# Optimization experiments

Measured on AMD Instinct MI355X. Metric: run time of the kernel, lower is better.

## Reference

```python
import jax, jax.numpy as jnp
import numpy as np

C = 16        # channel_n
HID = 128     # hidden width of 1x1 MLP
FIRE_RATE = 0.5
STEP_SIZE = 1.0
ALIVE_THRESH = 0.1
B, H, W = 16, 256, 256


def _perceive_kernel():
    # identity + Sobel filters, angle = 0.0 so cos=1, sin=0
    ident = np.outer([0.0, 1.0, 0.0], [0.0, 1.0, 0.0]).astype(np.float32)
    dxk = (np.outer([1.0, 2.0, 1.0], [-1.0, 0.0, 1.0]) / 8.0).astype(np.float32)
    dyk = dxk.T
    k3 = np.stack([ident, dxk, dyk], axis=-1)  # [3,3,3]
    # TF depthwise layout: out channel index = c*3 + k  -> tile over channels
    rhs = np.tile(k3, (1, 1, C)).reshape(3, 3, 1, 3 * C)  # HWIO, groups=C
    return jnp.asarray(rhs)


def _get_living_mask(x):
    alpha = x[:, :, :, 3:4]
    pooled = jax.lax.reduce_window(alpha, -jnp.inf, jax.lax.max,
                                   (1, 3, 3, 1), (1, 1, 1, 1), 'SAME')
    return pooled > ALIVE_THRESH


def _perceive(x):
    rhs = _perceive_kernel()
    return jax.lax.conv_general_dilated(
        x, rhs, window_strides=(1, 1), padding='SAME',
        dimension_numbers=('NHWC', 'HWIO', 'NHWC'),
        feature_group_count=C)  # [B,H,W,3C]


def setup_inputs() -> dict:
    key = jax.random.key(0)
    kx, kw1, kb1, ku = jax.random.split(key, 4)
    x = jax.random.normal(kx, (B, H, W, C), dtype=jnp.float32)
    # dmodel params: Conv2D(128,1,relu) then Conv2D(16,1,zeros init); use
    # random values for a meaningful numeric baseline
    W1 = jax.random.normal(kw1, (3 * C, HID), dtype=jnp.float32) * 0.1
    b1 = jax.random.normal(kb1, (HID,), dtype=jnp.float32) * 0.01
    W2 = jax.random.normal(jax.random.fold_in(key, 7), (HID, C), dtype=jnp.float32) * 0.1
    b2 = jnp.zeros((C,), dtype=jnp.float32)
    rand_u = jax.random.uniform(ku, (B, H, W, 1), dtype=jnp.float32)
    return {"x": x, "W1": W1, "b1": b1, "W2": W2, "b2": b2, "rand_u": rand_u}


def reference(x, W1, b1, W2, b2, rand_u):
    pre_life_mask = _get_living_mask(x)
    y = _perceive(x)                                         # [B,H,W,48]
    h = jax.nn.relu(jnp.einsum('bhwc,cd->bhwd', y, W1) + b1)  # [B,H,W,128]
    dx = (jnp.einsum('bhwd,dc->bhwc', h, W2) + b2) * STEP_SIZE
    update_mask = (rand_u <= FIRE_RATE).astype(x.dtype)
    x = x + dx * update_mask
    post_life_mask = _get_living_mask(x)
    life_mask = (pre_life_mask & post_life_mask).astype(x.dtype)
    return x * life_mask
```

## Files before the change

kernel.cpp:

```cpp
#include <hip/hip_runtime.h>


#define NC 16
#define NHID 128
#define NPIX (16 * 256 * 256)
#define MG 0.04f
#define MAXFIX 65536

typedef __attribute__((ext_vector_type(8))) short s8b;
typedef __attribute__((ext_vector_type(4))) float f4;

__device__ __forceinline__ unsigned short f2bf(float f) {
    union { float f; unsigned int u; } v; v.f = f;
    unsigned int r = (v.u + 0x7FFFu + ((v.u >> 16) & 1u)) >> 16;
    return (unsigned short)r;
}
__device__ __forceinline__ unsigned int pack2(float a, float b) {
    return (unsigned int)f2bf(a) | ((unsigned int)f2bf(b) << 16);
}

__global__ __launch_bounds__(256) void ca_prep(
    const float* __restrict__ W1, const float* __restrict__ b1,
    const float* __restrict__ W2, uint4* __restrict__ w1p, uint4* __restrict__ w2p)
{
    const int tid = threadIdx.x;
    if (blockIdx.x == 0) {
        for (int idx = tid; idx < 1024; idx += 256) {
            const int fid = idx >> 6, lane = idx & 63;
            const int k0 = fid >> 3, mt = fid & 7;
            const int q = lane >> 4, i = lane & 15;
            unsigned int u[4];
            #pragma unroll
            for (int jp = 0; jp < 4; ++jp) {
                int k = k0 * 32 + q * 8 + jp * 2;
                float v0 = (k < 48) ? W1[k * 128 + mt * 16 + i] : ((k == 48) ? b1[mt * 16 + i] : 0.f);
                k++;
                float v1 = (k < 48) ? W1[k * 128 + mt * 16 + i] : ((k == 48) ? b1[mt * 16 + i] : 0.f);
                u[jp] = pack2(v0, v1);
            }
            w1p[idx] = make_uint4(u[0], u[1], u[2], u[3]);
        }
    } else {
        for (int idx = tid; idx < 256; idx += 256) {
            const int k2 = idx >> 6, lane = idx & 63;
            const int q = lane >> 4, i = lane & 15;
            unsigned int u[4];
            #pragma unroll
            for (int jp = 0; jp < 4; ++jp) {
                const int k = k2 * 32 + q * 8 + jp * 2;
                u[jp] = pack2(W2[k * 16 + i], W2[(k + 1) * 16 + i]);
            }
            w2p[idx] = make_uint4(u[0], u[1], u[2], u[3]);
        }
    }
}

__global__ __launch_bounds__(256, 3) void ca_update(
    const float* __restrict__ x, const float* __restrict__ b2,
    const float* __restrict__ rand_u, const uint4* __restrict__ w1p,
    const uint4* __restrict__ w2p, float* __restrict__ out,
    float* __restrict__ ws_alpha, unsigned char* __restrict__ ws_pre,
    unsigned int* __restrict__ fix_cnt, unsigned int* __restrict__ fix_list)
{
    __shared__ __align__(16) float xw[18 * 18 * 20];
    __shared__ __align__(16) unsigned short yfs[4 * 2 * 528];
    __shared__ float lsr[256];

    const int tid  = threadIdx.x;
    const int lane = tid & 63;
    const int li   = lane & 15;
    const int lq   = lane >> 4;
    const int wv   = tid >> 6;
    const int tx   = tid & 15, ty = tid >> 4;
    const int w0 = blockIdx.x * 16, h0 = blockIdx.y * 16, bb = blockIdx.z;

    float b2v[4];
    #pragma unroll
    for (int r = 0; r < 4; ++r) b2v[r] = b2[lq * 4 + r];

    for (int i = tid; i < 324; i += 256) {
        const int ly = i / 18, lx = i - ly * 18;
        const int gh = h0 + ly - 1, gw = w0 + lx - 1;
        float4 v0, v1, v2, v3;
        if (gh >= 0 && gh < 256 && gw >= 0 && gw < 256) {
            const float4* p = (const float4*)(x + (((size_t)bb * 256 + gh) * 256 + gw) * NC);
            v0 = p[0]; v1 = p[1]; v2 = p[2]; v3 = p[3];
        } else {
            v0 = v1 = v2 = v3 = make_float4(0.f, 0.f, 0.f, 0.f);
        }
        float4* t = (float4*)(xw + i * 20);
        t[0] = v0; t[1] = v1; t[2] = v2; t[3] = v3;
    }
    const size_t gpix = ((size_t)bb * 256 + h0 + ty) * 256 + (w0 + tx);
    lsr[tid] = rand_u[gpix];
    __syncthreads();

    const int o_mm = ((ty + 0) * 18 + tx + 0) * 20, o_m0 = ((ty + 0) * 18 + tx + 1) * 20, o_mp = ((ty + 0) * 18 + tx + 2) * 20;
    const int o_0m = ((ty + 1) * 18 + tx + 0) * 20, o_cc = ((ty + 1) * 18 + tx + 1) * 20, o_0p = ((ty + 1) * 18 + tx + 2) * 20;
    const int o_pm = ((ty + 2) * 18 + tx + 0) * 20, o_p0 = ((ty + 2) * 18 + tx + 1) * 20, o_pp = ((ty + 2) * 18 + tx + 2) * 20;

    float am = xw[o_mm + 3];
    am = fmaxf(am, xw[o_m0 + 3]); am = fmaxf(am, xw[o_mp + 3]);
    am = fmaxf(am, xw[o_0m + 3]); am = fmaxf(am, xw[o_cc + 3]); am = fmaxf(am, xw[o_0p + 3]);
    am = fmaxf(am, xw[o_pm + 3]); am = fmaxf(am, xw[o_p0 + 3]); am = fmaxf(am, xw[o_pp + 3]);
    ws_pre[gpix] = (am > 0.1f) ? (unsigned char)1 : (unsigned char)0;

    unsigned int yu[24];
    #pragma unroll
    for (int cq = 0; cq < 4; ++cq) {
        const int co = cq * 4;
        float4 vmm = *(const float4*)(xw + o_mm + co); const float* pmm = (const float*)&vmm;
        float4 vm0 = *(const float4*)(xw + o_m0 + co); const float* pm0 = (const float*)&vm0;
        float4 vmp = *(const float4*)(xw + o_mp + co); const float* pmp = (const float*)&vmp;
        float4 v0m = *(const float4*)(xw + o_0m + co); const float* p0m = (const float*)&v0m;
        float4 vcc = *(const float4*)(xw + o_cc + co); const float* pcc = (const float*)&vcc;
        float4 v0p = *(const float4*)(xw + o_0p + co); const float* p0p = (const float*)&v0p;
        float4 vpm = *(const float4*)(xw + o_pm + co); const float* ppm = (const float*)&vpm;
        float4 vp0 = *(const float4*)(xw + o_p0 + co); const float* pp0 = (const float*)&vp0;
        float4 vpp = *(const float4*)(xw + o_pp + co); const float* ppp = (const float*)&vpp;
        float yl[12];
        #pragma unroll
        for (int cc = 0; cc < 4; ++cc) {
            const float xmm = pmm[cc], xm0 = pm0[cc], xmp = pmp[cc];
            const float x0m = p0m[cc], xcc = pcc[cc], x0p = p0p[cc];
            const float xpm = ppm[cc], xp0 = pp0[cc], xpp = ppp[cc];
            yl[cc * 3 + 0] = xcc;
            yl[cc * 3 + 1] = ((xmp - xmm) + 2.f * (x0p - x0m) + (xpp - xpm)) * 0.125f;
            yl[cc * 3 + 2] = ((xpm - xmm) + 2.f * (xp0 - xm0) + (xpp - xmp)) * 0.125f;
        }
        #pragma unroll
        for (int m2 = 0; m2 < 6; ++m2) yu[cq * 6 + m2] = pack2(yl[2 * m2], yl[2 * m2 + 1]);
    }

    float4 xcr[4];
    #pragma unroll
    for (int s4 = 0; s4 < 4; ++s4)
        xcr[s4] = *(const float4*)(xw + ((wv * 4 + s4 + 1) * 18 + li + 1) * 20 + lq * 4);
    __syncthreads();

    for (int i = tid; i < 1280; i += 256)
        ((uint4*)xw)[i] = w1p[i];
    __syncthreads();

    const unsigned short* wl = (const unsigned short*)xw;
    unsigned short* yfw = yfs + wv * (2 * 528);

    const int srcA = li + (lq & 1) * 32;
    const int srcB = srcA + 16;
    const bool hiq = (lq >= 2);

    #pragma unroll
    for (int s = 0; s < 4; ++s) {
        const int t = wv * 4 + s;
        if ((ty & 3) == s) {
            #pragma unroll
            for (int q = 0; q < 4; ++q)
                *(uint4*)(yfw + (q * 16 + tx) * 8) = make_uint4(yu[q * 4], yu[q * 4 + 1], yu[q * 4 + 2], yu[q * 4 + 3]);
            *(uint4*)(yfw + 528 + (0 * 16 + tx) * 8) = make_uint4(yu[16], yu[17], yu[18], yu[19]);
            *(uint4*)(yfw + 528 + (1 * 16 + tx) * 8) = make_uint4(yu[20], yu[21], yu[22], yu[23]);
            *(uint4*)(yfw + 528 + (2 * 16 + tx) * 8) = make_uint4(0x3F80u, 0u, 0u, 0u);
            *(uint4*)(yfw + 528 + (3 * 16 + tx) * 8) = make_uint4(0u, 0u, 0u, 0u);
        }
        const s8b ya0 = *(const s8b*)(yfw + lane * 8);
        const s8b ya1 = *(const s8b*)(yfw + 528 + lane * 8);

        f4 acc1[8];
        #pragma unroll
        for (int mt = 0; mt < 8; ++mt) { f4 z = {0.f, 0.f, 0.f, 0.f}; acc1[mt] = z; }
        #pragma unroll
        for (int mt = 0; mt < 8; ++mt) {
            const s8b wf = *(const s8b*)(wl + mt * 512 + lane * 8);
            acc1[mt] = __builtin_amdgcn_mfma_f32_16x16x32_bf16(wf, ya0, acc1[mt], 0, 0, 0);
        }
        #pragma unroll
        for (int mt = 0; mt < 8; ++mt) {
            const s8b wf = *(const s8b*)(wl + (8 + mt) * 512 + lane * 8);
            acc1[mt] = __builtin_amdgcn_mfma_f32_16x16x32_bf16(wf, ya1, acc1[mt], 0, 0, 0);
        }

        f4 acc2[2];
        { f4 z = {0.f, 0.f, 0.f, 0.f}; acc2[0] = z; acc2[1] = z; }
        #pragma unroll
        for (int k2 = 0; k2 < 4; ++k2) {
            const f4 aE = acc1[2 * k2], aO = acc1[2 * k2 + 1];
            const unsigned int e0 = pack2(fmaxf(aE[0], 0.f), fmaxf(aE[1], 0.f));
            const unsigned int e1 = pack2(fmaxf(aE[2], 0.f), fmaxf(aE[3], 0.f));
            const unsigned int o0 = pack2(fmaxf(aO[0], 0.f), fmaxf(aO[1], 0.f));
            const unsigned int o1 = pack2(fmaxf(aO[2], 0.f), fmaxf(aO[3], 0.f));
            const unsigned int vE0A = (unsigned int)__shfl((int)e0, srcA, 64);
            const unsigned int vE1A = (unsigned int)__shfl((int)e1, srcA, 64);
            const unsigned int vO0A = (unsigned int)__shfl((int)o0, srcA, 64);
            const unsigned int vO1A = (unsigned int)__shfl((int)o1, srcA, 64);
            const unsigned int vE0B = (unsigned int)__shfl((int)e0, srcB, 64);
            const unsigned int vE1B = (unsigned int)__shfl((int)e1, srcB, 64);
            const unsigned int vO0B = (unsigned int)__shfl((int)o0, srcB, 64);
            const unsigned int vO1B = (unsigned int)__shfl((int)o1, srcB, 64);
            union { uint4 u; s8b v; } hb;
            hb.u = make_uint4(hiq ? vO0A : vE0A, hiq ? vO1A : vE1A,
                              hiq ? vO0B : vE0B, hiq ? vO1B : vE1B);
            const s8b w2fr = *(const s8b*)(wl + 8192 + k2 * 512 + lane * 8);
            acc2[k2 >> 1] = __builtin_amdgcn_mfma_f32_16x16x32_bf16(w2fr, hb.v, acc2[k2 >> 1], 0, 0, 0);
        }

        const float um = (lsr[t * 16 + li] <= 0.5f) ? 1.f : 0.f;
        const size_t gp = ((size_t)bb * 256 + h0 + t) * 256 + (w0 + li);
        const float4 xc = xcr[s];
        f4 nx;
        nx[0] = fmaf(acc2[0][0] + acc2[1][0] + b2v[0], um, xc.x);
        nx[1] = fmaf(acc2[0][1] + acc2[1][1] + b2v[1], um, xc.y);
        nx[2] = fmaf(acc2[0][2] + acc2[1][2] + b2v[2], um, xc.z);
        nx[3] = fmaf(acc2[0][3] + acc2[1][3] + b2v[3], um, xc.w);
        __builtin_nontemporal_store(nx, (f4*)out + gp * 4 + lq);
        if (lq == 0) {
            ws_alpha[gp] = nx[3];
            if (um != 0.f && fabsf(nx[3] - 0.1f) <= MG) {
                unsigned int idx = atomicAdd(fix_cnt, 1u);
                if (idx < MAXFIX) fix_list[idx] = (unsigned int)gp;
            }
        }
    }
}

__global__ __launch_bounds__(64) void ca_fix(
    const float* __restrict__ x, const float* __restrict__ W1,
    const float* __restrict__ b1, const float* __restrict__ W2,
    const float* __restrict__ b2,
    const unsigned int* __restrict__ fix_cnt, const unsigned int* __restrict__ fix_list,
    float* __restrict__ ws_alpha)
{
    __shared__ float ysh[48];
    const int lane = threadIdx.x;
    unsigned int n = *fix_cnt;
    if (n > MAXFIX) n = MAXFIX;
    for (unsigned int e = blockIdx.x; e < n; e += gridDim.x) {
        const unsigned int pix = fix_list[e];
        const int bb = pix >> 16, h = (pix >> 8) & 255, w = pix & 255;
        if (lane < 48) {
            const int c = lane / 3, j = lane - c * 3;
            float v = 0.f;
            #pragma unroll
            for (int dy = 0; dy < 3; ++dy) {
                #pragma unroll
                for (int dxx = 0; dxx < 3; ++dxx) {
                    const int hh = h + dy - 1, ww = w + dxx - 1;
                    if (hh < 0 || hh >= 256 || ww < 0 || ww >= 256) continue;
                    const float f = x[(((size_t)bb * 256 + hh) * 256 + ww) * 16 + c];
                    float wgt;
                    if (j == 0) wgt = (dy == 1 && dxx == 1) ? 1.f : 0.f;
                    else if (j == 1) wgt = ((dy == 1) ? 2.f : 1.f) * (float)(dxx - 1) * 0.125f;
                    else wgt = ((dxx == 1) ? 2.f : 1.f) * (float)(dy - 1) * 0.125f;
                    v = fmaf(f, wgt, v);
                }
            }
            ysh[lane] = v;
        }
        __syncthreads();
        float dot = 0.f;
        #pragma unroll
        for (int t = 0; t < 2; ++t) {
            const int d = t * 64 + lane;
            float a = b1[d];
            #pragma unroll
            for (int k = 0; k < 48; ++k)
                a = fmaf(ysh[k], W1[k * 128 + d], a);
            dot = fmaf(fmaxf(a, 0.f), W2[d * 16 + 3], dot);
        }
        #pragma unroll
        for (int off = 32; off > 0; off >>= 1)
            dot += __shfl_down(dot, off, 64);
        if (lane == 0)
            ws_alpha[pix] = x[(size_t)pix * 16 + 3] + dot + b2[3];
        __syncthreads();
    }
}

__global__ __launch_bounds__(256) void ca_mask(
    const float* __restrict__ alpha, const unsigned char* __restrict__ pre,
    float* __restrict__ out)
{
    __shared__ float at[18 * 20];
    const int tid = threadIdx.x;
    const int w0 = blockIdx.x * 16, h0 = blockIdx.y * 16, bb = blockIdx.z;
    for (int i = tid; i < 324; i += 256) {
        const int ly = i / 18, lx = i - ly * 18;
        const int gh = h0 + ly - 1, gw = w0 + lx - 1;
        float v = 0.f;
        if (gh >= 0 && gh < 256 && gw >= 0 && gw < 256)
            v = alpha[((size_t)bb * 256 + gh) * 256 + gw];
        at[ly * 20 + lx] = v;
    }
    __syncthreads();
    const int txx = tid & 15, tyy = tid >> 4;
    float m = at[tyy * 20 + txx];
    m = fmaxf(m, at[tyy * 20 + txx + 1]); m = fmaxf(m, at[tyy * 20 + txx + 2]);
    m = fmaxf(m, at[(tyy + 1) * 20 + txx]); m = fmaxf(m, at[(tyy + 1) * 20 + txx + 1]); m = fmaxf(m, at[(tyy + 1) * 20 + txx + 2]);
    m = fmaxf(m, at[(tyy + 2) * 20 + txx]); m = fmaxf(m, at[(tyy + 2) * 20 + txx + 1]); m = fmaxf(m, at[(tyy + 2) * 20 + txx + 2]);
    const size_t gp = ((size_t)bb * 256 + h0 + tyy) * 256 + (w0 + txx);
    const bool alive = (m > 0.1f) && pre[gp];
    if (!alive) {
        float4* po = (float4*)(out + gp * 16);
        const float4 z = make_float4(0.f, 0.f, 0.f, 0.f);
        po[0] = z; po[1] = z; po[2] = z; po[3] = z;
    }
}

extern "C" void kernel_launch(void* const* d_in, const int* in_sizes, int n_in,
                              void* d_out, int out_size, void* d_ws, size_t ws_size,
                              hipStream_t stream) {
    (void)in_sizes; (void)n_in; (void)out_size; (void)ws_size;
    const float* x  = (const float*)d_in[0];
    const float* W1 = (const float*)d_in[1];
    const float* b1 = (const float*)d_in[2];
    const float* W2 = (const float*)d_in[3];
    const float* b2 = (const float*)d_in[4];
    const float* ru = (const float*)d_in[5];
    float* out = (float*)d_out;

    char* ws = (char*)d_ws;
    float* ws_alpha       = (float*)ws;
    unsigned char* ws_pre = (unsigned char*)(ws + (size_t)NPIX * 4);
    uint4* w1p            = (uint4*)(ws + (size_t)NPIX * 5);
    uint4* w2p            = w1p + 1024;
    unsigned int* fix_cnt = (unsigned int*)(ws + (size_t)NPIX * 5 + 20480);
    unsigned int* fix_list= fix_cnt + 4;

    (void)hipMemsetAsync(fix_cnt, 0, sizeof(unsigned int), stream);
    ca_prep<<<2, 256, 0, stream>>>(W1, b1, W2, w1p, w2p);
    dim3 g(16, 16, 16);
    ca_update<<<g, 256, 0, stream>>>(x, b2, ru, w1p, w2p, out, ws_alpha, ws_pre, fix_cnt, fix_list);
    ca_fix<<<4096, 64, 0, stream>>>(x, W1, b1, W2, b2, fix_cnt, fix_list, ws_alpha);
    ca_mask<<<g, 256, 0, stream>>>(ws_alpha, ws_pre, out);
}
```

Baseline: 340.2 us.

## Read stencil neighbors directly from global memory instead of LDS halo tile

Removes the 18x18x20 float shared-memory halo tile. Each thread now loads its nine neighbor pixels straight from global memory through the cache, and the center pixel and rand_u are re-read from global in the epilogue. The W1 weight copy into shared memory moves to the kernel start, which drops one barrier and a large chunk of LDS, so more blocks can be resident per CU. The cost is roughly nine times more global or cache load traffic per pixel, instead of one halo-tile load per block.

```diff
diff --git a/kernel.cpp b/kernel.cpp
--- a/kernel.cpp
+++ b/kernel.cpp
@@ -62,9 +62,8 @@
     float* __restrict__ ws_alpha, unsigned char* __restrict__ ws_pre,
     unsigned int* __restrict__ fix_cnt, unsigned int* __restrict__ fix_list)
 {
-    __shared__ __align__(16) float xw[18 * 18 * 20];
+    __shared__ __align__(16) uint4 wsm[1280];
     __shared__ __align__(16) unsigned short yfs[4 * 2 * 528];
-    __shared__ float lsr[256];
 
     const int tid  = threadIdx.x;
     const int lane = tid & 63;
@@ -74,50 +73,57 @@
     const int tx   = tid & 15, ty = tid >> 4;
     const int w0 = blockIdx.x * 16, h0 = blockIdx.y * 16, bb = blockIdx.z;
 
+    for (int i = tid; i < 1280; i += 256)
+        wsm[i] = w1p[i];
+
     float b2v[4];
     #pragma unroll
     for (int r = 0; r < 4; ++r) b2v[r] = b2[lq * 4 + r];
 
-    for (int i = tid; i < 324; i += 256) {
-        const int ly = i / 18, lx = i - ly * 18;
-        const int gh = h0 + ly - 1, gw = w0 + lx - 1;
-        float4 v0, v1, v2, v3;
-        if (gh >= 0 && gh < 256 && gw >= 0 && gw < 256) {
-            const float4* p = (const float4*)(x + (((size_t)bb * 256 + gh) * 256 + gw) * NC);
-            v0 = p[0]; v1 = p[1]; v2 = p[2]; v3 = p[3];
-        } else {
-            v0 = v1 = v2 = v3 = make_float4(0.f, 0.f, 0.f, 0.f);
-        }
-        float4* t = (float4*)(xw + i * 20);
-        t[0] = v0; t[1] = v1; t[2] = v2; t[3] = v3;
-    }
-    const size_t gpix = ((size_t)bb * 256 + h0 + ty) * 256 + (w0 + tx);
-    lsr[tid] = rand_u[gpix];
-    __syncthreads();
-
-    const int o_mm = ((ty + 0) * 18 + tx + 0) * 20, o_m0 = ((ty + 0) * 18 + tx + 1) * 20, o_mp = ((ty + 0) * 18 + tx + 2) * 20;
-    const int o_0m = ((ty + 1) * 18 + tx + 0) * 20, o_cc = ((ty + 1) * 18 + tx + 1) * 20, o_0p = ((ty + 1) * 18 + tx + 2) * 20;
-    const int o_pm = ((ty + 2) * 18 + tx + 0) * 20, o_p0 = ((ty + 2) * 18 + tx + 1) * 20, o_pp = ((ty + 2) * 18 + tx + 2) * 20;
-
-    float am = xw[o_mm + 3];
-    am = fmaxf(am, xw[o_m0 + 3]); am = fmaxf(am, xw[o_mp + 3]);
-    am = fmaxf(am, xw[o_0m + 3]); am = fmaxf(am, xw[o_cc + 3]); am = fmaxf(am, xw[o_0p + 3]);
-    am = fmaxf(am, xw[o_pm + 3]); am = fmaxf(am, xw[o_p0 + 3]); am = fmaxf(am, xw[o_pp + 3]);
-    ws_pre[gpix] = (am > 0.1f) ? (unsigned char)1 : (unsigned char)0;
+    const int gh = h0 + ty, gw = w0 + tx;
+    const size_t gpix = ((size_t)bb * 256 + gh) * 256 + gw;
+    const float* xb = x + (size_t)bb * 256 * 256 * NC;
+
+    bool nv[3][3];
+    size_t nb[3][3];
+    #pragma unroll
+    for (int dy = 0; dy < 3; ++dy) {
+        const int hh = gh + dy - 1;
+        const bool hv = (hh >= 0) && (hh < 256);
+        #pragma unroll
+        for (int dxx = 0; dxx < 3; ++dxx) {
+            const int ww = gw + dxx - 1;
+            nv[dy][dxx] = hv && (ww >= 0) && (ww < 256);
+            nb[dy][dxx] = ((size_t)(hv ? hh : 0) * 256 + (size_t)((ww >= 0 && ww < 256) ? ww : 0)) * NC;
+        }
+    }
 
     unsigned int yu[24];
+    float am = 0.f;
     #pragma unroll
     for (int cq = 0; cq < 4; ++cq) {
         const int co = cq * 4;
-        float4 vmm = *(const float4*)(xw + o_mm + co); const float* pmm = (const float*)&vmm;
-        float4 vm0 = *(const float4*)(xw + o_m0 + co); const float* pm0 = (const float*)&vm0;
-        float4 vmp = *(const float4*)(xw + o_mp + co); const float* pmp = (const float*)&vmp;
-        float4 v0m = *(const float4*)(xw + o_0m + co); const float* p0m = (const float*)&v0m;
-        float4 vcc = *(const float4*)(xw + o_cc + co); const float* pcc = (const float*)&vcc;
-        float4 v0p = *(const float4*)(xw + o_0p + co); const float* p0p = (const float*)&v0p;
-        float4 vpm = *(const float4*)(xw + o_pm + co); const float* ppm = (const float*)&vpm;
-        float4 vp0 = *(const float4*)(xw + o_p0 + co); const float* pp0 = (const float*)&vp0;
-        float4 vpp = *(const float4*)(xw + o_pp + co); const float* ppp = (const float*)&vpp;
+        const float4 z4 = make_float4(0.f, 0.f, 0.f, 0.f);
+        float4 vmm = nv[0][0] ? *(const float4*)(xb + nb[0][0] + co) : z4;
+        float4 vm0 = nv[0][1] ? *(const float4*)(xb + nb[0][1] + co) : z4;
+        float4 vmp = nv[0][2] ? *(const float4*)(xb + nb[0][2] + co) : z4;
+        float4 v0m = nv[1][0] ? *(const float4*)(xb + nb[1][0] + co) : z4;
+        float4 vcc = nv[1][1] ? *(const float4*)(xb + nb[1][1] + co) : z4;
+        float4 v0p = nv[1][2] ? *(const float4*)(xb + nb[1][2] + co) : z4;
+        float4 vpm = nv[2][0] ? *(const float4*)(xb + nb[2][0] + co) : z4;
+        float4 vp0 = nv[2][1] ? *(const float4*)(xb + nb[2][1] + co) : z4;
+        float4 vpp = nv[2][2] ? *(const float4*)(xb + nb[2][2] + co) : z4;
+        if (cq == 0) {
+            am = vmm.w;
+            am = fmaxf(am, vm0.w); am = fmaxf(am, vmp.w);
+            am = fmaxf(am, v0m.w); am = fmaxf(am, vcc.w); am = fmaxf(am, v0p.w);
+            am = fmaxf(am, vpm.w); am = fmaxf(am, vp0.w); am = fmaxf(am, vpp.w);
+        }
+        const float* pmm = (const float*)&vmm; const float* pm0 = (const float*)&vm0;
+        const float* pmp = (const float*)&vmp; const float* p0m = (const float*)&v0m;
+        const float* pcc = (const float*)&vcc; const float* p0p = (const float*)&v0p;
+        const float* ppm = (const float*)&vpm; const float* pp0 = (const float*)&vp0;
+        const float* ppp = (const float*)&vpp;
         float yl[12];
         #pragma unroll
         for (int cc = 0; cc < 4; ++cc) {
@@ -131,18 +137,11 @@
         #pragma unroll
         for (int m2 = 0; m2 < 6; ++m2) yu[cq * 6 + m2] = pack2(yl[2 * m2], yl[2 * m2 + 1]);
     }
-
-    float4 xcr[4];
-    #pragma unroll
-    for (int s4 = 0; s4 < 4; ++s4)
-        xcr[s4] = *(const float4*)(xw + ((wv * 4 + s4 + 1) * 18 + li + 1) * 20 + lq * 4);
+    ws_pre[gpix] = (am > 0.1f) ? (unsigned char)1 : (unsigned char)0;
+
     __syncthreads();
 
-    for (int i = tid; i < 1280; i += 256)
-        ((uint4*)xw)[i] = w1p[i];
-    __syncthreads();
-
-    const unsigned short* wl = (const unsigned short*)xw;
+    const unsigned short* wl = (const unsigned short*)wsm;
     unsigned short* yfw = yfs + wv * (2 * 528);
 
     const int srcA = li + (lq & 1) * 32;
@@ -202,14 +201,14 @@
             acc2[k2 >> 1] = __builtin_amdgcn_mfma_f32_16x16x32_bf16(w2fr, hb.v, acc2[k2 >> 1], 0, 0, 0);
         }
 
-        const float um = (lsr[t * 16 + li] <= 0.5f) ? 1.f : 0.f;
         const size_t gp = ((size_t)bb * 256 + h0 + t) * 256 + (w0 + li);
-        const float4 xc = xcr[s];
+        const float um = (rand_u[gp] <= 0.5f) ? 1.f : 0.f;
+        const f4 xc = *((const f4*)x + gp * 4 + lq);
         f4 nx;
-        nx[0] = fmaf(acc2[0][0] + acc2[1][0] + b2v[0], um, xc.x);
-        nx[1] = fmaf(acc2[0][1] + acc2[1][1] + b2v[1], um, xc.y);
-        nx[2] = fmaf(acc2[0][2] + acc2[1][2] + b2v[2], um, xc.z);
-        nx[3] = fmaf(acc2[0][3] + acc2[1][3] + b2v[3], um, xc.w);
+        nx[0] = fmaf(acc2[0][0] + acc2[1][0] + b2v[0], um, xc[0]);
+        nx[1] = fmaf(acc2[0][1] + acc2[1][1] + b2v[1], um, xc[1]);
+        nx[2] = fmaf(acc2[0][2] + acc2[1][2] + b2v[2], um, xc[2]);
+        nx[3] = fmaf(acc2[0][3] + acc2[1][3] + b2v[3], um, xc[3]);
         __builtin_nontemporal_store(nx, (f4*)out + gp * 4 + lq);
         if (lq == 0) {
             ws_alpha[gp] = nx[3];
```

Measured after the change: 413.4 us. 1.22x slower.
